# Performance work log

Hardware: AMD Instinct MI355X
Metric: run time of the kernel (lower is better)

Reference implementation:

```python
import jax, jax.numpy as jnp
import numpy as np

B, F, H, E, V, L = 16384, 512, 512, 128, 128, 10  # batch, feature, hidden, embed, vocab, msg len


def setup_inputs() -> dict:
    key = jax.random.key(0)
    ks = jax.random.split(key, 8)
    def s(k, shape, scale=0.05):
        return jax.random.normal(k, shape, jnp.float32) * scale
    return {
        "inputs": jax.random.normal(ks[0], (B, F), jnp.float32),
        "W_vh": s(ks[1], (F, H)),
        "b_vh": jnp.zeros((H,), jnp.float32),
        "gru_kernel": s(ks[2], (E, 3 * H)),          # input kernel [E, 3H] (z|r|h order like keras)
        "gru_rec_kernel": s(ks[3], (H, 3 * H)),      # recurrent kernel [H, 3H]
        "gru_bias": jnp.zeros((2, 3 * H), jnp.float32),  # [input_bias; recurrent_bias], reset_after=True
        "W_out": s(ks[4], (H, V)),
        "b_out": jnp.zeros((V,), jnp.float32),
        "embedding": s(ks[5], (V, E)),
    }


def gru_cell(x, h, Wk, Uk, bias):
    # keras GRUCell with reset_after=True:
    #   matrix_x = x @ Wk + b_i ; matrix_h = h @ Uk + b_r (split z|r|h)
    xz = x @ Wk + bias[0]
    hz = h @ Uk + bias[1]
    xi, xr, xh = jnp.split(xz, 3, axis=1)
    hi, hr, hh_inner = jnp.split(hz, 3, axis=1)
    z = jax.nn.sigmoid(xi + hi)
    r = jax.nn.sigmoid(xr + hr)
    hh = jnp.tanh(xh + r * hh_inner)
    return z * h + (1.0 - z) * hh


def reference(inputs, W_vh, b_vh, gru_kernel, gru_rec_kernel, gru_bias, W_out, b_out, embedding):
    h0 = jnp.tanh(inputs @ W_vh + b_vh)                      # vision_to_hidden (tanh)
    x0 = jnp.zeros((inputs.shape[0], E), inputs.dtype)       # initial cell input = zeros

    def step(carry, _):
        x, h = carry
        h_t = gru_cell(x, h, gru_kernel, gru_rec_kernel, gru_bias)
        logp = jax.nn.log_softmax(h_t @ W_out + b_out, axis=1)    # [B, V]
        ent = -jnp.sum(logp * jnp.exp(logp), axis=1)              # [B]
        sym = jnp.argmax(logp, axis=1)                            # training=False path -> argmax
        chosen = jnp.take_along_axis(logp, sym[:, None], axis=1)[:, 0]
        x_next = embedding[sym]                                   # next cell input
        return (x_next, h_t), (sym, chosen, ent)

    (_, h_t), (syms, chosens, ents) = jax.lax.scan(step, (x0, h0), None, length=L)
    sequence = syms.T.astype(jnp.float32)        # [B, L]
    logits = chosens.T                            # [B, L] log-prob of chosen symbol
    entropy = jnp.mean(ents.T, axis=1)            # [B]
    message_length = jnp.full_like(entropy, float(L))
    return sequence, logits, entropy, message_length, h_t
```

## Files before the change

### kernel.cpp

```cpp
#include <hip/hip_runtime.h>
#include <math.h>

namespace {

constexpr int Bsz  = 16384;
constexpr int Fdim = 512;
constexpr int Hdim = 512;
constexpr int Vdim = 128;
constexpr int Lmsg = 10;
constexpr int H3   = 3 * Hdim;

constexpr float SPLIT_SC  = 32.0f;
constexpr float SPLIT_INV = 0.03125f;

typedef _Float16 half4v __attribute__((ext_vector_type(4)));
typedef _Float16 half8v __attribute__((ext_vector_type(8)));
typedef float    f32x4  __attribute__((ext_vector_type(4)));

__device__ __forceinline__ float sigm(float x) { return 1.0f / (1.0f + __expf(-x)); }

__global__ void k_embk(const float* __restrict__ emb, const float* __restrict__ gk,
                       const float* __restrict__ bias0, float* __restrict__ emb_k,
                       int* __restrict__ sym) {
    const int gid = blockIdx.x * 256 + threadIdx.x;
    const int v = gid / H3, j = gid - v * H3;
    float acc = bias0[j];
    const float* er = emb + v * 128;
    #pragma unroll 4
    for (int e = 0; e < 128; ++e) acc = fmaf(er[e], gk[e * H3 + j], acc);
    emb_k[gid] = acc;
    if (gid < Bsz) sym[gid] = 0;
}

__global__ void k_usplit(const float* __restrict__ guk,
                         _Float16* __restrict__ uthi, _Float16* __restrict__ utlo) {
    const int gid = blockIdx.x * 256 + threadIdx.x;
    const int j = gid >> 9, k = gid & 511;
    const float u = guk[(size_t)k * H3 + j];
    const _Float16 hi = (_Float16)u;
    uthi[gid] = hi;
    utlo[gid] = (_Float16)((u - (float)hi) * SPLIT_SC);
}

__global__ void k_osplit(const float* __restrict__ Wout,
                         _Float16* __restrict__ wthi, _Float16* __restrict__ wtlo) {
    const int gid = blockIdx.x * 256 + threadIdx.x;
    const int j = gid >> 9, k = gid & 511;
    const float u = Wout[(size_t)k * Vdim + j];
    const _Float16 hi = (_Float16)u;
    wthi[gid] = hi;
    wtlo[gid] = (_Float16)((u - (float)hi) * SPLIT_SC);
}

__global__ __launch_bounds__(256, 2) void k_vision(const float* __restrict__ A,
                                                   const float* __restrict__ W,
                                                   const float* __restrict__ bias,
                                                   _Float16* __restrict__ hiP,
                                                   _Float16* __restrict__ loP) {
    __shared__ float As[16][132];
    __shared__ float Bs[16][64];
    const int tid = threadIdx.x;
    const int tx = tid & 15, ty = tid >> 4;
    const int r0 = blockIdx.y * 128, c0 = blockIdx.x * 64;

    const int arow = tid >> 2;
    const int acol = (tid & 3) * 4;
    const int bk   = tid >> 4;
    const int bcol = (tid & 15) * 4;

    const float* Abase = A + r0 * Fdim;
    float acc[8][4] = {};

    float4 pa0 = *(const float4*)(Abase + arow * Fdim + acol);
    float4 pa1 = *(const float4*)(Abase + (arow + 64) * Fdim + acol);
    float4 pb  = *(const float4*)(W + bk * Hdim + c0 + bcol);

    for (int kc = 0; kc < Fdim / 16; ++kc) {
        __syncthreads();
        As[acol + 0][arow] = pa0.x;  As[acol + 1][arow] = pa0.y;
        As[acol + 2][arow] = pa0.z;  As[acol + 3][arow] = pa0.w;
        As[acol + 0][arow + 64] = pa1.x;  As[acol + 1][arow + 64] = pa1.y;
        As[acol + 2][arow + 64] = pa1.z;  As[acol + 3][arow + 64] = pa1.w;
        *(float4*)&Bs[bk][bcol] = pb;
        __syncthreads();
        if (kc + 1 < Fdim / 16) {
            const int k0 = (kc + 1) * 16;
            pa0 = *(const float4*)(Abase + arow * Fdim + k0 + acol);
            pa1 = *(const float4*)(Abase + (arow + 64) * Fdim + k0 + acol);
            pb  = *(const float4*)(W + (k0 + bk) * Hdim + c0 + bcol);
        }
        #pragma unroll
        for (int k = 0; k < 16; ++k) {
            const float4 a0 = *(const float4*)&As[k][ty * 8];
            const float4 a1 = *(const float4*)&As[k][ty * 8 + 4];
            const float4 b  = *(const float4*)&Bs[k][tx * 4];
            const float av[8] = {a0.x,a0.y,a0.z,a0.w,a1.x,a1.y,a1.z,a1.w};
            const float bv[4] = {b.x,b.y,b.z,b.w};
            #pragma unroll
            for (int i = 0; i < 8; ++i)
                #pragma unroll
                for (int n = 0; n < 4; ++n)
                    acc[i][n] = fmaf(av[i], bv[n], acc[i][n]);
        }
    }
    const float4 bb = *(const float4*)(bias + c0 + tx * 4);
    #pragma unroll
    for (int i = 0; i < 8; ++i) {
        const int r = r0 + ty * 8 + i;
        float o0 = tanhf(acc[i][0] + bb.x);
        float o1 = tanhf(acc[i][1] + bb.y);
        float o2 = tanhf(acc[i][2] + bb.z);
        float o3 = tanhf(acc[i][3] + bb.w);
        half4v hv, lv;
        hv.x = (_Float16)o0; lv.x = (_Float16)((o0 - (float)hv.x) * SPLIT_SC);
        hv.y = (_Float16)o1; lv.y = (_Float16)((o1 - (float)hv.y) * SPLIT_SC);
        hv.z = (_Float16)o2; lv.z = (_Float16)((o2 - (float)hv.z) * SPLIT_SC);
        hv.w = (_Float16)o3; lv.w = (_Float16)((o3 - (float)hv.w) * SPLIT_SC);
        *(half4v*)(hiP + (size_t)r * Hdim + c0 + tx * 4) = hv;
        *(half4v*)(loP + (size_t)r * Hdim + c0 + tx * 4) = lv;
    }
}

__global__ __launch_bounds__(256, 2) void k_gru(
    const _Float16* __restrict__ hiIn, const _Float16* __restrict__ loIn,
    const _Float16* __restrict__ uthi, const _Float16* __restrict__ utlo,
    const float* __restrict__ gbias,
    const float* __restrict__ emb_k,
    const int* __restrict__ sym,
    int step,
    _Float16* __restrict__ hiOut, _Float16* __restrict__ loOut,
    float* __restrict__ hF) {

    __shared__ __align__(16) char smem[2 * 28672];
    const int tid = threadIdx.x;
    const int l = tid & 63, w = tid >> 6;

    const int bid = blockIdx.x;
    const int swz = (bid & 7) * 256 + (bid >> 3);
    const int rb = swz >> 4, cb = swz & 15;
    const int m0 = rb * 128, c0 = cb * 32;

    const char* gsrc[7];
    int loff[7];
    {
        int n = 0;
        #pragma unroll
        for (int s0 = 0; s0 < 4; ++s0) {
            const int s = w + s0 * 4;
            const _Float16* pl = (s < 8) ? hiIn : loIn;
            const int seg = (s < 8) ? s : s - 8;
            const int grow = seg * 16 + (l >> 2);
            const int slot = (l & 3) ^ (grow & 3);
            gsrc[n] = (const char*)(pl + (size_t)(m0 + grow) * Hdim) + slot * 16;
            loff[n] = ((s < 8) ? 0 : 8192) + seg * 1024;
            ++n;
        }
        #pragma unroll
        for (int s0 = 0; s0 < 3; ++s0) {
            const int s = w + s0 * 4;
            const _Float16* pl = (s < 6) ? uthi : utlo;
            const int seg = (s < 6) ? s : s - 6;
            const int jrow = seg * 16 + (l >> 2);
            const int g = jrow >> 5, jl = jrow & 31;
            const int slot = (l & 3) ^ (jrow & 3);
            gsrc[n] = (const char*)(pl + (size_t)(g * Hdim + c0 + jl) * Hdim) + slot * 16;
            loff[n] = 16384 + ((s < 6) ? 0 : 6144) + seg * 1024;
            ++n;
        }
    }

    f32x4 acc[2][2][3] = {};

    {
        char* lb = smem;
        #pragma unroll
        for (int i = 0; i < 7; ++i)
            __builtin_amdgcn_global_load_lds(
                (const __attribute__((address_space(1))) void*)(gsrc[i]),
                (__attribute__((address_space(3))) void*)(lb + loff[i]), 16, 0, 0);
    }

    const int fr = l & 15;
    const int kb_lane = l >> 4;
    const int sw_rd = ((kb_lane ^ (l & 3)) << 4);

    for (int kc = 0; kc < 16; ++kc) {
        __syncthreads();
        if (kc < 15) {
            char* lb = smem + ((kc + 1) & 1) * 28672;
            const int kbyt = (kc + 1) * 64;
            #pragma unroll
            for (int i = 0; i < 7; ++i)
                __builtin_amdgcn_global_load_lds(
                    (const __attribute__((address_space(1))) void*)(gsrc[i] + kbyt),
                    (__attribute__((address_space(3))) void*)(lb + loff[i]), 16, 0, 0);
        }
        const char* lb = smem + (kc & 1) * 28672;

        half8v ahi[2], alo[2], ahid[2];
        #pragma unroll
        for (int mf = 0; mf < 2; ++mf) {
            const int r = w * 32 + mf * 16 + fr;
            const int byt = r * 64 + sw_rd;
            ahi[mf]  = *(const half8v*)(lb + byt);
            alo[mf]  = *(const half8v*)(lb + 8192 + byt);
            ahid[mf] = ahi[mf] * (_Float16)SPLIT_INV;
        }
        #pragma unroll
        for (int g = 0; g < 3; ++g) {
            #pragma unroll
            for (int nf = 0; nf < 2; ++nf) {
                const int jrow = g * 32 + nf * 16 + fr;
                const int byt = jrow * 64 + sw_rd;
                half8v bhi  = *(const half8v*)(lb + 16384 + byt);
                half8v blo  = *(const half8v*)(lb + 22528 + byt);
                half8v bhid = bhi * (_Float16)SPLIT_INV;
                #pragma unroll
                for (int mf = 0; mf < 2; ++mf) {
                    acc[mf][nf][g] = __builtin_amdgcn_mfma_f32_16x16x32_f16(
                        ahi[mf], bhi, acc[mf][nf][g], 0, 0, 0);
                    acc[mf][nf][g] = __builtin_amdgcn_mfma_f32_16x16x32_f16(
                        ahid[mf], blo, acc[mf][nf][g], 0, 0, 0);
                    acc[mf][nf][g] = __builtin_amdgcn_mfma_f32_16x16x32_f16(
                        alo[mf], bhid, acc[mf][nf][g], 0, 0, 0);
                }
            }
        }
    }

    const float* bias1 = gbias + H3;
    float b1z[2], b1r[2], b1h[2];
    #pragma unroll
    for (int nf = 0; nf < 2; ++nf) {
        const int jg = c0 + nf * 16 + fr;
        b1z[nf] = bias1[jg];
        b1r[nf] = bias1[Hdim + jg];
        b1h[nf] = bias1[2 * Hdim + jg];
    }
    #pragma unroll
    for (int mf = 0; mf < 2; ++mf) {
        #pragma unroll
        for (int q = 0; q < 4; ++q) {
            const int r = m0 + w * 32 + mf * 16 + kb_lane * 4 + q;
            const float* xrow = (step == 0) ? gbias : (emb_k + (size_t)sym[r] * H3);
            #pragma unroll
            for (int nf = 0; nf < 2; ++nf) {
                const int jg = c0 + nf * 16 + fr;
                const float xz = xrow[jg];
                const float xr_ = xrow[Hdim + jg];
                const float xh = xrow[2 * Hdim + jg];
                const float az = acc[mf][nf][0][q];
                const float ar = acc[mf][nf][1][q];
                const float ah = acc[mf][nf][2][q];
                const size_t idx = (size_t)r * Hdim + jg;
                const float hold = (float)hiIn[idx] + (float)loIn[idx] * SPLIT_INV;
                const float z  = sigm(xz + b1z[nf] + az);
                const float rr = sigm(xr_ + b1r[nf] + ar);
                const float hh = tanhf(xh + rr * (b1h[nf] + ah));
                const float o = z * hold + (1.0f - z) * hh;
                const _Float16 oh = (_Float16)o;
                hiOut[idx] = oh;
                loOut[idx] = (_Float16)((o - (float)oh) * SPLIT_SC);
                if (hF) hF[idx] = o;
            }
        }
    }
}

__global__ __launch_bounds__(256, 2) void k_out(
    const _Float16* __restrict__ hiP, const _Float16* __restrict__ loP,
    const _Float16* __restrict__ wthi, const _Float16* __restrict__ wtlo,
    const float* __restrict__ bout, int step,
    float* __restrict__ seqO, float* __restrict__ logO,
    float* __restrict__ entO, float* __restrict__ lenO,
    int* __restrict__ symO) {

    __shared__ __align__(16) char smem[2 * 24576];
    const int tid = threadIdx.x;
    const int l = tid & 63, w = tid >> 6;
    const int r0 = blockIdx.x * 64;

    const char* gsrc[6];
    int loff[6];
    {
        #pragma unroll
        for (int i = 0; i < 6; ++i) {
            const int s = w + i * 4;
            if (s < 8) {
                const _Float16* pl = (s < 4) ? hiP : loP;
                const int seg = (s < 4) ? s : s - 4;
                const int grow = seg * 16 + (l >> 2);
                const int slot = (l & 3) ^ (grow & 3);
                gsrc[i] = (const char*)(pl + (size_t)(r0 + grow) * Hdim) + slot * 16;
                loff[i] = ((s < 4) ? 0 : 4096) + seg * 1024;
            } else {
                const int t = s - 8;
                const _Float16* pl = (t < 8) ? wthi : wtlo;
                const int seg = (t < 8) ? t : t - 8;
                const int grow = seg * 16 + (l >> 2);
                const int slot = (l & 3) ^ (grow & 3);
                gsrc[i] = (const char*)(pl + (size_t)grow * Hdim) + slot * 16;
                loff[i] = 8192 + ((t < 8) ? 0 : 8192) + seg * 1024;
            }
        }
    }

    f32x4 acc[8] = {};

    {
        char* lb = smem;
        #pragma unroll
        for (int i = 0; i < 6; ++i)
            __builtin_amdgcn_global_load_lds(
                (const __attribute__((address_space(1))) void*)(gsrc[i]),
                (__attribute__((address_space(3))) void*)(lb + loff[i]), 16, 0, 0);
    }

    const int fr = l & 15, kb = l >> 4;
    const int sw_rd = ((kb ^ (l & 3)) << 4);

    for (int kc = 0; kc < 16; ++kc) {
        __syncthreads();
        if (kc < 15) {
            char* lb = smem + ((kc + 1) & 1) * 24576;
            const int kbyt = (kc + 1) * 64;
            #pragma unroll
            for (int i = 0; i < 6; ++i)
                __builtin_amdgcn_global_load_lds(
                    (const __attribute__((address_space(1))) void*)(gsrc[i] + kbyt),
                    (__attribute__((address_space(3))) void*)(lb + loff[i]), 16, 0, 0);
        }
        const char* lb = smem + (kc & 1) * 24576;

        const int abyt = (w * 16 + fr) * 64 + sw_rd;
        half8v ahi  = *(const half8v*)(lb + abyt);
        half8v alo  = *(const half8v*)(lb + 4096 + abyt);
        half8v ahid = ahi * (_Float16)SPLIT_INV;
        #pragma unroll
        for (int nf = 0; nf < 8; ++nf) {
            const int bbyt = (nf * 16 + fr) * 64 + sw_rd;
            half8v bhi  = *(const half8v*)(lb + 8192 + bbyt);
            half8v blo  = *(const half8v*)(lb + 16384 + bbyt);
            half8v bhid = bhi * (_Float16)SPLIT_INV;
            acc[nf] = __builtin_amdgcn_mfma_f32_16x16x32_f16(ahi,  bhi,  acc[nf], 0, 0, 0);
            acc[nf] = __builtin_amdgcn_mfma_f32_16x16x32_f16(ahid, blo,  acc[nf], 0, 0, 0);
            acc[nf] = __builtin_amdgcn_mfma_f32_16x16x32_f16(alo,  bhid, acc[nf], 0, 0, 0);
        }
    }

    float bo[8];
    #pragma unroll
    for (int nf = 0; nf < 8; ++nf) bo[nf] = bout[nf * 16 + fr];

    #pragma unroll
    for (int q = 0; q < 4; ++q) {
        float vals[8];
        #pragma unroll
        for (int nf = 0; nf < 8; ++nf) vals[nf] = acc[nf][q] + bo[nf];

        float vmax = vals[0]; int vidx = fr;
        #pragma unroll
        for (int nf = 1; nf < 8; ++nf)
            if (vals[nf] > vmax) { vmax = vals[nf]; vidx = nf * 16 + fr; }
        #pragma unroll
        for (int off = 1; off < 16; off <<= 1) {
            const float ov = __shfl_xor(vmax, off);
            const int   oi = __shfl_xor(vidx, off);
            if (ov > vmax || (ov == vmax && oi < vidx)) { vmax = ov; vidx = oi; }
        }

        float s = 0.0f, t2 = 0.0f;
        #pragma unroll
        for (int nf = 0; nf < 8; ++nf) {
            const float d = vals[nf] - vmax;
            const float e = __expf(d);
            s += e; t2 = fmaf(e, d, t2);
        }
        #pragma unroll
        for (int off = 1; off < 16; off <<= 1) {
            s  += __shfl_xor(s, off);
            t2 += __shfl_xor(t2, off);
        }

        if (fr == 0) {
            const int rg = r0 + w * 16 + kb * 4 + q;
            const float logS = logf(s);
            const float ent  = logS - t2 / s;
            seqO[rg * Lmsg + step] = (float)vidx;
            logO[rg * Lmsg + step] = -logS;
            symO[rg] = vidx;
            if (step == 0) { entO[rg] = ent * (1.0f / Lmsg); lenO[rg] = (float)Lmsg; }
            else           { entO[rg] += ent * (1.0f / Lmsg); }
        }
    }
}

}

extern "C" void kernel_launch(void* const* d_in, const int* in_sizes, int n_in,
                              void* d_out, int out_size, void* d_ws, size_t ws_size,
                              hipStream_t stream) {
    (void)in_sizes; (void)n_in; (void)out_size; (void)ws_size;

    const float* inputs = (const float*)d_in[0];
    const float* W_vh   = (const float*)d_in[1];
    const float* b_vh   = (const float*)d_in[2];
    const float* gk     = (const float*)d_in[3];
    const float* guk    = (const float*)d_in[4];
    const float* gbias  = (const float*)d_in[5];
    const float* Wout   = (const float*)d_in[6];
    const float* bout   = (const float*)d_in[7];
    const float* emb    = (const float*)d_in[8];

    float* out  = (float*)d_out;
    float* seqO = out;
    float* logO = out + (size_t)Bsz * Lmsg;
    float* entO = out + (size_t)2 * Bsz * Lmsg;
    float* lenO = entO + Bsz;
    float* hF   = lenO + Bsz;

    char* wsb = (char*)d_ws;
    const size_t PLANE = (size_t)Bsz * Hdim * sizeof(_Float16);
    _Float16* pH[2] = { (_Float16*)(wsb),             (_Float16*)(wsb + 2 * PLANE) };
    _Float16* pL[2] = { (_Float16*)(wsb + PLANE),     (_Float16*)(wsb + 3 * PLANE) };
    _Float16* uthi  = (_Float16*)(wsb + 4 * PLANE);
    _Float16* utlo  = uthi + (size_t)H3 * Hdim;
    _Float16* wthi  = utlo + (size_t)H3 * Hdim;
    _Float16* wtlo  = wthi + (size_t)Vdim * Hdim;
    float*    emb_k = (float*)(wtlo + (size_t)Vdim * Hdim);
    int*      sym   = (int*)(emb_k + (size_t)Vdim * H3);

    k_embk  <<<dim3(Vdim * H3 / 256), 256, 0, stream>>>(emb, gk, gbias, emb_k, sym);
    k_usplit<<<dim3(H3 * Hdim / 256), 256, 0, stream>>>(guk, uthi, utlo);
    k_osplit<<<dim3(Vdim * Hdim / 256), 256, 0, stream>>>(Wout, wthi, wtlo);
    k_vision<<<dim3(Hdim / 64, Bsz / 128), 256, 0, stream>>>(inputs, W_vh, b_vh, pH[0], pL[0]);

    for (int t = 0; t < Lmsg; ++t) {
        const int rd = t & 1, wr = (t + 1) & 1;
        k_gru<<<dim3((Bsz / 128) * (Hdim / 32)), 256, 0, stream>>>(
            pH[rd], pL[rd], uthi, utlo, gbias, emb_k, sym, t,
            pH[wr], pL[wr], (t == Lmsg - 1) ? hF : nullptr);
        k_out<<<dim3(Bsz / 64), 256, 0, stream>>>(
            pH[wr], pL[wr], wthi, wtlo, bout, t, seqO, logO, entO, lenO, sym);
    }
}
```

Before: 1.497 ms.

## Move vision projection to split-fp16 MFMA GEMM with async LDS loads

Replaces the FP32 SIMT tiled GEMM for the initial hidden projection with a matrix-core kernel. Inputs and W_vh are first split into fp16 hi/lo planes, and three MFMA products emulate fp32 accuracy. Tiles are staged through double-buffered LDS using global_load_lds with XOR swizzle and a block-index swizzle. This targets the slow FP32 vision GEMM, at the cost of extra split kernels and extra memory traffic for the split input planes.

After: 1.387 ms. -7.3%, faster.

```diff
diff --git a/kernel.cpp b/kernel.cpp
--- a/kernel.cpp
+++ b/kernel.cpp
@@ -32,92 +32,128 @@
     if (gid < Bsz) sym[gid] = 0;
 }
 
-__global__ void k_usplit(const float* __restrict__ guk,
-                         _Float16* __restrict__ uthi, _Float16* __restrict__ utlo) {
+__global__ void k_split(const float* __restrict__ src,
+                        _Float16* __restrict__ dhi, _Float16* __restrict__ dlo,
+                        int N) {
     const int gid = blockIdx.x * 256 + threadIdx.x;
     const int j = gid >> 9, k = gid & 511;
-    const float u = guk[(size_t)k * H3 + j];
+    const float u = src[(size_t)k * N + j];
     const _Float16 hi = (_Float16)u;
-    uthi[gid] = hi;
-    utlo[gid] = (_Float16)((u - (float)hi) * SPLIT_SC);
-}
-
-__global__ void k_osplit(const float* __restrict__ Wout,
-                         _Float16* __restrict__ wthi, _Float16* __restrict__ wtlo) {
-    const int gid = blockIdx.x * 256 + threadIdx.x;
-    const int j = gid >> 9, k = gid & 511;
-    const float u = Wout[(size_t)k * Vdim + j];
-    const _Float16 hi = (_Float16)u;
-    wthi[gid] = hi;
-    wtlo[gid] = (_Float16)((u - (float)hi) * SPLIT_SC);
-}
-
-__global__ __launch_bounds__(256, 2) void k_vision(const float* __restrict__ A,
-                                                   const float* __restrict__ W,
-                                                   const float* __restrict__ bias,
-                                                   _Float16* __restrict__ hiP,
-                                                   _Float16* __restrict__ loP) {
-    __shared__ float As[16][132];
-    __shared__ float Bs[16][64];
+    dhi[gid] = hi;
+    dlo[gid] = (_Float16)((u - (float)hi) * SPLIT_SC);
+}
+
+__global__ void k_asplit(const float* __restrict__ x,
+                         _Float16* __restrict__ hi, _Float16* __restrict__ lo) {
+    const size_t i = ((size_t)blockIdx.x * 256 + threadIdx.x) * 4;
+    const float4 v = *(const float4*)(x + i);
+    half4v h, l;
+    h.x = (_Float16)v.x; l.x = (_Float16)((v.x - (float)h.x) * SPLIT_SC);
+    h.y = (_Float16)v.y; l.y = (_Float16)((v.y - (float)h.y) * SPLIT_SC);
+    h.z = (_Float16)v.z; l.z = (_Float16)((v.z - (float)h.z) * SPLIT_SC);
+    h.w = (_Float16)v.w; l.w = (_Float16)((v.w - (float)h.w) * SPLIT_SC);
+    *(half4v*)(hi + i) = h;
+    *(half4v*)(lo + i) = l;
+}
+
+__global__ __launch_bounds__(256, 2) void k_vision2(
+    const _Float16* __restrict__ aHi, const _Float16* __restrict__ aLo,
+    const _Float16* __restrict__ wvhi, const _Float16* __restrict__ wvlo,
+    const float* __restrict__ bias,
+    _Float16* __restrict__ hiP, _Float16* __restrict__ loP) {
+
+    __shared__ __align__(16) char smem[2 * 24576];
     const int tid = threadIdx.x;
-    const int tx = tid & 15, ty = tid >> 4;
-    const int r0 = blockIdx.y * 128, c0 = blockIdx.x * 64;
-
-    const int arow = tid >> 2;
-    const int acol = (tid & 3) * 4;
-    const int bk   = tid >> 4;
-    const int bcol = (tid & 15) * 4;
-
-    const float* Abase = A + r0 * Fdim;
-    float acc[8][4] = {};
-
-    float4 pa0 = *(const float4*)(Abase + arow * Fdim + acol);
-    float4 pa1 = *(const float4*)(Abase + (arow + 64) * Fdim + acol);
-    float4 pb  = *(const float4*)(W + bk * Hdim + c0 + bcol);
-
-    for (int kc = 0; kc < Fdim / 16; ++kc) {
+    const int l = tid & 63, w = tid >> 6;
+
+    const int bid = blockIdx.x;
+    const int swz = (bid & 7) * 128 + (bid >> 3);
+    const int rb = swz >> 2, cb = swz & 3;
+    const int r0 = rb * 64, c0 = cb * 128;
+
+    const char* gsrc[6];
+    int loff[6];
+    {
+        #pragma unroll
+        for (int i = 0; i < 6; ++i) {
+            const int s = w + i * 4;
+            if (s < 8) {
+                const _Float16* pl = (s < 4) ? aHi : aLo;
+                const int seg = s & 3;
+                const int grow = seg * 16 + (l >> 2);
+                const int slot = (l & 3) ^ (grow & 3);
+                gsrc[i] = (const char*)(pl + (size_t)(r0 + grow) * Hdim) + slot * 16;
+                loff[i] = ((s < 4) ? 0 : 4096) + seg * 1024;
+            } else {
+                const int t = s - 8;
+                const _Float16* pl = (t < 8) ? wvhi : wvlo;
+                const int seg = t & 7;
+                const int grow = seg * 16 + (l >> 2);
+                const int slot = (l & 3) ^ (grow & 3);
+                gsrc[i] = (const char*)(pl + (size_t)(c0 + grow) * Hdim) + slot * 16;
+                loff[i] = 8192 + ((t < 8) ? 0 : 8192) + seg * 1024;
+            }
+        }
+    }
+
+    f32x4 acc[8] = {};
+
+    {
+        char* lb = smem;
+        #pragma unroll
+        for (int i = 0; i < 6; ++i)
+            __builtin_amdgcn_global_load_lds(
+                (const __attribute__((address_space(1))) void*)(gsrc[i]),
+                (__attribute__((address_space(3))) void*)(lb + loff[i]), 16, 0, 0);
+    }
+
+    const int fr = l & 15, kb = l >> 4;
+    const int sw_rd = ((kb ^ (l & 3)) << 4);
+
+    for (int kc = 0; kc < 16; ++kc) {
         __syncthreads();
-        As[acol + 0][arow] = pa0.x;  As[acol + 1][arow] = pa0.y;
-        As[acol + 2][arow] = pa0.z;  As[acol + 3][arow] = pa0.w;
-        As[acol + 0][arow + 64] = pa1.x;  As[acol + 1][arow + 64] = pa1.y;
-        As[acol + 2][arow + 64] = pa1.z;  As[acol + 3][arow + 64] = pa1.w;
-        *(float4*)&Bs[bk][bcol] = pb;
-        __syncthreads();
-        if (kc + 1 < Fdim / 16) {
-            const int k0 = (kc + 1) * 16;
-            pa0 = *(const float4*)(Abase + arow * Fdim + k0 + acol);
-            pa1 = *(const float4*)(Abase + (arow + 64) * Fdim + k0 + acol);
-            pb  = *(const float4*)(W + (k0 + bk) * Hdim + c0 + bcol);
-        }
-        #pragma unroll
-        for (int k = 0; k < 16; ++k) {
-            const float4 a0 = *(const float4*)&As[k][ty * 8];
-            const float4 a1 = *(const float4*)&As[k][ty * 8 + 4];
-            const float4 b  = *(const float4*)&Bs[k][tx * 4];
-            const float av[8] = {a0.x,a0.y,a0.z,a0.w,a1.x,a1.y,a1.z,a1.w};
-            const float bv[4] = {b.x,b.y,b.z,b.w};
+        if (kc < 15) {
+            char* lb = smem + ((kc + 1) & 1) * 24576;
+            const int kbyt = (kc + 1) * 64;
             #pragma unroll
-            for (int i = 0; i < 8; ++i)
-                #pragma unroll
-                for (int n = 0; n < 4; ++n)
-                    acc[i][n] = fmaf(av[i], bv[n], acc[i][n]);
-        }
-    }
-    const float4 bb = *(const float4*)(bias + c0 + tx * 4);
-    #pragma unroll
-    for (int i = 0; i < 8; ++i) {
-        const int r = r0 + ty * 8 + i;
-        float o0 = tanhf(acc[i][0] + bb.x);
-        float o1 = tanhf(acc[i][1] + bb.y);
-        float o2 = tanhf(acc[i][2] + bb.z);
-        float o3 = tanhf(acc[i][3] + bb.w);
-        half4v hv, lv;
-        hv.x = (_Float16)o0; lv.x = (_Float16)((o0 - (float)hv.x) * SPLIT_SC);
-        hv.y = (_Float16)o1; lv.y = (_Float16)((o1 - (float)hv.y) * SPLIT_SC);
-        hv.z = (_Float16)o2; lv.z = (_Float16)((o2 - (float)hv.z) * SPLIT_SC);
-        hv.w = (_Float16)o3; lv.w = (_Float16)((o3 - (float)hv.w) * SPLIT_SC);
-        *(half4v*)(hiP + (size_t)r * Hdim + c0 + tx * 4) = hv;
-        *(half4v*)(loP + (size_t)r * Hdim + c0 + tx * 4) = lv;
+            for (int i = 0; i < 6; ++i)
+                __builtin_amdgcn_global_load_lds(
+                    (const __attribute__((address_space(1))) void*)(gsrc[i] + kbyt),
+                    (__attribute__((address_space(3))) void*)(lb + loff[i]), 16, 0, 0);
+        }
+        const char* lb = smem + (kc & 1) * 24576;
+
+        const int abyt = (w * 16 + fr) * 64 + sw_rd;
+        half8v ahi  = *(const half8v*)(lb + abyt);
+        half8v alo  = *(const half8v*)(lb + 4096 + abyt);
+        half8v ahid = ahi * (_Float16)SPLIT_INV;
+        #pragma unroll
+        for (int nf = 0; nf < 8; ++nf) {
+            const int bbyt = (nf * 16 + fr) * 64 + sw_rd;
+            half8v bhi  = *(const half8v*)(lb + 8192 + bbyt);
+            half8v blo  = *(const half8v*)(lb + 16384 + bbyt);
+            half8v bhid = bhi * (_Float16)SPLIT_INV;
+            acc[nf] = __builtin_amdgcn_mfma_f32_16x16x32_f16(ahi,  bhi,  acc[nf], 0, 0, 0);
+            acc[nf] = __builtin_amdgcn_mfma_f32_16x16x32_f16(ahid, blo,  acc[nf], 0, 0, 0);
+            acc[nf] = __builtin_amdgcn_mfma_f32_16x16x32_f16(alo,  bhid, acc[nf], 0, 0, 0);
+        }
+    }
+
+    float bo[8];
+    #pragma unroll
+    for (int nf = 0; nf < 8; ++nf) bo[nf] = bias[c0 + nf * 16 + fr];
+
+    #pragma unroll
+    for (int q = 0; q < 4; ++q) {
+        const int r = r0 + w * 16 + kb * 4 + q;
+        #pragma unroll
+        for (int nf = 0; nf < 8; ++nf) {
+            const float o = tanhf(acc[nf][q] + bo[nf]);
+            const _Float16 oh = (_Float16)o;
+            const size_t idx = (size_t)r * Hdim + c0 + nf * 16 + fr;
+            hiP[idx] = oh;
+            loP[idx] = (_Float16)((o - (float)oh) * SPLIT_SC);
+        }
     }
 }
 
@@ -423,17 +459,24 @@
     const size_t PLANE = (size_t)Bsz * Hdim * sizeof(_Float16);
     _Float16* pH[2] = { (_Float16*)(wsb),             (_Float16*)(wsb + 2 * PLANE) };
     _Float16* pL[2] = { (_Float16*)(wsb + PLANE),     (_Float16*)(wsb + 3 * PLANE) };
+    _Float16* aHi   = pH[1];
+    _Float16* aLo   = pL[1];
     _Float16* uthi  = (_Float16*)(wsb + 4 * PLANE);
     _Float16* utlo  = uthi + (size_t)H3 * Hdim;
     _Float16* wthi  = utlo + (size_t)H3 * Hdim;
     _Float16* wtlo  = wthi + (size_t)Vdim * Hdim;
-    float*    emb_k = (float*)(wtlo + (size_t)Vdim * Hdim);
+    _Float16* wvhi  = wtlo + (size_t)Vdim * Hdim;
+    _Float16* wvlo  = wvhi + (size_t)Hdim * Hdim;
+    float*    emb_k = (float*)(wvlo + (size_t)Hdim * Hdim);
     int*      sym   = (int*)(emb_k + (size_t)Vdim * H3);
 
     k_embk  <<<dim3(Vdim * H3 / 256), 256, 0, stream>>>(emb, gk, gbias, emb_k, sym);
-    k_usplit<<<dim3(H3 * Hdim / 256), 256, 0, stream>>>(guk, uthi, utlo);
-    k_osplit<<<dim3(Vdim * Hdim / 256), 256, 0, stream>>>(Wout, wthi, wtlo);
-    k_vision<<<dim3(Hdim / 64, Bsz / 128), 256, 0, stream>>>(inputs, W_vh, b_vh, pH[0], pL[0]);
+    k_split <<<dim3(H3 * Hdim / 256), 256, 0, stream>>>(guk, uthi, utlo, H3);
+    k_split <<<dim3(Vdim * Hdim / 256), 256, 0, stream>>>(Wout, wthi, wtlo, Vdim);
+    k_split <<<dim3(Hdim * Hdim / 256), 256, 0, stream>>>(W_vh, wvhi, wvlo, Hdim);
+    k_asplit<<<dim3(Bsz * Fdim / 1024), 256, 0, stream>>>(inputs, aHi, aLo);
+    k_vision2<<<dim3((Bsz / 64) * 4), 256, 0, stream>>>(aHi, aLo, wvhi, wvlo, b_vh,
+                                                        pH[0], pL[0]);
 
     for (int t = 0; t < Lmsg; ++t) {
         const int rd = t & 1, wr = (t + 1) & 1;
```
